# Kernel tuning notes

Hardware: AMD Instinct MI355X
Metric: run time of the kernel (lower is better)

Reference implementation:

```python
import jax, jax.numpy as jnp
import numpy as np

B, L, K, G, C, S = 1024, 32, 8, 8, 128, 32
D_IN = 2 * L + K + S  # masked z (L) + mask (L) + target (K) + shared (S)
TAU = 1.0
EPS = 1e-5
NEG_INF = -1e9  # stands in for torch's -9e15 diagonal fill; sigmoid(-1e9)=0


def setup_inputs() -> dict:
    key = jax.random.key(0)
    ks = jax.random.split(key, 24)
    eye = jnp.eye(K, dtype=bool)
    kaiming = lambda k, shape: jax.random.uniform(k, shape, jnp.float32, -1.0, 1.0) * np.sqrt(6.0 / shape[-1])
    return {
        "z_sample": jax.random.normal(ks[0], (B, L), jnp.float32),
        "target": jax.random.randint(ks[1], (B,), 0, K),
        "z_mean": jax.random.normal(ks[2], (B, L), jnp.float32),
        "z_logstd": 0.1 * jax.random.normal(ks[3], (B, L), jnp.float32),
        "z_shared": jax.random.normal(ks[4], (B, S), jnp.float32),
        "u_gumbel": jax.random.uniform(ks[5], (B, L, K), jnp.float32),
        "u_adj": jax.random.uniform(ks[6], (B, G, K, K), jnp.float32),
        "target_params": 0.1 * jax.random.normal(ks[7], (L, K), jnp.float32),
        "enco_theta": jnp.where(eye, NEG_INF, jax.random.normal(ks[8], (K, K), jnp.float32)),
        "enco_gamma": jnp.where(eye, NEG_INF, jax.random.normal(ks[9], (K, K), jnp.float32)),
        "W1": kaiming(ks[10], (L, C, D_IN)),
        "b1": jnp.zeros((L, C), jnp.float32),
        "gn1_w": jnp.ones((L, C), jnp.float32),
        "gn1_b": jnp.zeros((L, C), jnp.float32),
        "W2": kaiming(ks[11], (L, C, C)),
        "b2": jnp.zeros((L, C), jnp.float32),
        "gn2_w": jnp.ones((L, C), jnp.float32),
        "gn2_b": jnp.zeros((L, C), jnp.float32),
        "W3": 0.01 * jax.random.normal(ks[12], (L, 2, C), jnp.float32),
        "b3": jnp.zeros((L, 2), jnp.float32),
        "tanh_scale": jnp.zeros((L, 2), jnp.float32),
    }


def _mv_linear(x, W, b):
    # x: [B,G,L,d_in], W: [L,d_out,d_in] -> [B,G,L,d_out]  (per-latent independent linear)
    return jnp.einsum("bgld,lhd->bglh", x, W) + b


def _mv_groupnorm(x, w, b):
    # GroupNorm(L groups over L*C channels) == per-(sample, latent) normalization over C
    mu = x.mean(-1, keepdims=True)
    var = ((x - mu) ** 2).mean(-1, keepdims=True)
    return (x - mu) * jax.lax.rsqrt(var + EPS) * w + b


def reference(z_sample, target, z_mean, z_logstd, z_shared, u_gumbel, u_adj,
              target_params, enco_theta, enco_gamma,
              W1, b1, gn1_w, gn1_b, W2, b2, gn2_w, gn2_b, W3, b3, tanh_scale):
    dt = z_sample.dtype
    target_oh = jax.nn.one_hot(target, K, dtype=dt)  # [B,K]

    # hard gumbel-softmax with straight-through estimator: psi assigns latents to causal vars
    g = -jnp.log(-jnp.log(u_gumbel + 1e-10) + 1e-10)
    soft = jax.nn.softmax((target_params[None] + g) / TAU, axis=-1)  # [B,L,K]
    hard = jax.nn.one_hot(jnp.argmax(soft, axis=-1), K, dtype=dt)
    psi = hard + soft - jax.lax.stop_gradient(soft)  # [B,L,K]

    # ENCO graph sampling: edge prob = sigmoid(theta)*sigmoid(gamma), Bernoulli samples
    edge_prob = jax.nn.sigmoid(enco_theta) * jax.nn.sigmoid(enco_gamma)  # [K,K]
    adj = (u_adj < edge_prob[None, None]).astype(dt)  # [B,G,K,K], adj[k,l]=1: k->l

    # latent-level parent mask: mask[b,g,i,j]=1 iff latent j is a parent of latent i
    latent_mask = jnp.einsum("bil,bgkl,bjk->bgij", psi, adj, psi)  # [B,G,L,L]
    latent_mask = latent_mask * (1.0 - jnp.eye(L, dtype=dt))

    # per-latent network input: [masked parents, mask, intervention indicator, shared]
    z_masked = latent_mask * z_sample[:, None, None, :]                        # [B,G,L,L]
    t_inp = jnp.broadcast_to((psi * target_oh[:, None, :])[:, None], (B, G, L, K))
    zs = jnp.broadcast_to(z_shared[:, None, None, :], (B, G, L, S))
    s_inp = jnp.concatenate([z_masked, latent_mask, t_inp, zs], axis=-1)       # [B,G,L,D_IN]

    h = jax.nn.silu(_mv_groupnorm(_mv_linear(s_inp, W1, b1), gn1_w, gn1_b))
    h = jax.nn.silu(_mv_groupnorm(_mv_linear(h, W2, b2), gn2_w, gn2_b))
    h = _mv_linear(h, W3, b3)                                                  # [B,G,L,2]
    sc = jnp.exp(tanh_scale)                                                   # [L,2]
    h = jnp.tanh(h / sc) * sc                                                  # MultivarStableTanh
    prior_mean, prior_logstd = h[..., 0], h[..., 1]                            # [B,G,L]

    # KL(q(z) || p(z)) per latent, averaged over graph samples, summed over latents
    var_q = jnp.exp(2.0 * z_logstd)[:, None]                                   # [B,1,L]
    kld = (prior_logstd - z_logstd[:, None]
           + (var_q + (z_mean[:, None] - prior_mean) ** 2) / (2.0 * jnp.exp(2.0 * prior_logstd))
           - 0.5)                                                              # [B,G,L]
    return kld.mean(axis=1).sum(axis=-1)                                       # [B]
```

## Files before the change

### kernel.cpp

```cpp
#include <hip/hip_runtime.h>
#include <hip/hip_bf16.h>

#define B_DIM 1024
#define L_DIM 32
#define K_DIM 8
#define G_DIM 8
#define C_DIM 128
#define S_DIM 32
#define DIN   104

typedef __bf16  bf16x8 __attribute__((ext_vector_type(8)));
typedef float   f32x4  __attribute__((ext_vector_type(4)));

union frag_u { uint4 u; bf16x8 v; };

static __device__ __forceinline__ unsigned int pk2(float a, float b) {
    __hip_bfloat162 h = __float22bfloat162_rn(make_float2(a, b));
    union { __hip_bfloat162 h; unsigned int u; } v; v.h = h; return v.u;
}
static __device__ __forceinline__ bf16x8 ld_frag(const unsigned short* p) {
    frag_u t; t.u = *(const uint4*)p; return t.v;
}

__global__ __launch_bounds__(256) void prep_kernel(
    const float* __restrict__ u_gumbel,
    const float* __restrict__ u_adj,
    const float* __restrict__ target_params,
    const float* __restrict__ enco_theta,
    const float* __restrict__ enco_gamma,
    const int*   __restrict__ target,
    const float* __restrict__ W1,
    const float* __restrict__ W2,
    float*       __restrict__ out,
    unsigned char* __restrict__ cvarpk,
    unsigned int*  __restrict__ wsmask,
    unsigned short* __restrict__ wscr)
{
    const int t = threadIdx.x;
    if (blockIdx.x >= 1024) {
        int gtid  = (blockIdx.x - 1024) * 256 + t;
        int lane  = gtid & 63;
        int ks    = (gtid >> 6) & 3;
        int mt    = (gtid >> 8) & 3;
        int wm    = (gtid >> 10) & 1;
        int l     = (gtid >> 11) & 31;
        int which = gtid >> 16;
        int m  = 16 * (4 * wm + mt) + (lane & 15);
        int k0 = ks * 32 + (lane >> 4) * 8;
        uint4 o;
        if (which == 0) {
            if (k0 >= 104) {
                o = make_uint4(0u, 0u, 0u, 0u);
            } else {
                const float* p = W1 + (size_t)l * 13312 + m * 104 + k0;
                float4 a = *(const float4*)p, bq = *(const float4*)(p + 4);
                o = make_uint4(pk2(a.x, a.y), pk2(a.z, a.w), pk2(bq.x, bq.y), pk2(bq.z, bq.w));
            }
        } else {
            const float* p = W2 + (size_t)l * 16384 + m * 128 + k0;
            float4 a = *(const float4*)p, bq = *(const float4*)(p + 4);
            o = make_uint4(pk2(a.x, a.y), pk2(a.z, a.w), pk2(bq.x, bq.y), pk2(bq.z, bq.w));
        }
        *(uint4*)(wscr + (size_t)gtid * 8) = o;
        return;
    }

    __shared__ double ep[64];
    __shared__ unsigned char cv8[32];
    __shared__ unsigned long long adjb[8];
    const int b = blockIdx.x;
    if (t < 64) {
        double th = (double)enco_theta[t];
        double ga = (double)enco_gamma[t];
        ep[t] = (1.0 / (1.0 + exp(-th))) * (1.0 / (1.0 + exp(-ga)));
    }
    if (t == 0) out[b] = 0.0f;
    __syncthreads();

    {
        const int l = t >> 3, k = t & 7;
        double u = (double)u_gumbel[b * 256 + t];
        double g = -log(-log(u + 1e-10) + 1e-10);
        double v = (double)target_params[t] + g;
        int bk = k;
        #pragma unroll
        for (int off = 1; off < 8; off <<= 1) {
            double ov = __shfl_xor(v, off, 64);
            int   obk = __shfl_xor(bk, off, 64);
            if (ov > v || (ov == v && obk < bk)) { v = ov; bk = obk; }
        }
        if (k == 0) {
            int tg = target[b];
            unsigned char pkd = (unsigned char)(bk | ((bk == tg) ? 8 : 0));
            cvarpk[b * 32 + l] = pkd;
            cv8[l] = pkd;
        }
    }
    {
        const int wv = t >> 6, lane = t & 63;
        #pragma unroll
        for (int q = 0; q < 2; ++q) {
            int gg = wv + 4 * q;
            double u = (double)u_adj[b * 512 + gg * 64 + lane];
            unsigned long long m = __ballot(u < ep[lane]);
            if (lane == 0) adjb[gg] = m;
        }
    }
    __syncthreads();

    {
        const int g = t >> 5, l = t & 31;
        int lam = cv8[l] & 7;
        unsigned long long bits = adjb[g] >> lam;
        unsigned int mask = 0u;
        #pragma unroll
        for (int j = 0; j < 32; ++j) {
            int kap = cv8[j] & 7;
            mask |= ((unsigned int)(bits >> (kap * 8)) & 1u) << j;
        }
        mask &= ~(1u << l);
        wsmask[l * 8192 + b * 8 + g] = mask;
    }
}

__global__ __launch_bounds__(256, 2) void fused_kernel(
    const float* __restrict__ z_sample,
    const float* __restrict__ z_mean,
    const float* __restrict__ z_logstd,
    const float* __restrict__ z_shared,
    const float* __restrict__ pb1,
    const float* __restrict__ g1w,
    const float* __restrict__ g1b,
    const float* __restrict__ pb2,
    const float* __restrict__ g2w,
    const float* __restrict__ g2b,
    const float* __restrict__ W3,
    const float* __restrict__ pb3,
    const float* __restrict__ tsc,
    const unsigned short* __restrict__ wscr,
    const unsigned char*  __restrict__ cvarpk,
    const unsigned int*   __restrict__ wsmask,
    float* __restrict__ out)
{
    __shared__ __align__(16) unsigned short XH[128][136];
    __shared__ float2 gnA[2][128];
    __shared__ float2 gnB[2][128];
    __shared__ float p_g1w[128], p_g1b[128], p_g2w[128], p_g2b[128], p_b1[128], p_b2[128];
    __shared__ float p_w3[2][128];
    __shared__ float p_b3[2], p_ts[2];
    __shared__ __align__(16) unsigned long long cvs[16][4];

    const int tid  = threadIdx.x;
    const int w    = tid >> 6, lane = tid & 63;
    const int lo   = lane & 15, hi = lane >> 4;
    const int wm   = w & 1, wn = w >> 1;
    const int l    = blockIdx.x & 31;
    const int grp  = blockIdx.x >> 5;

    const unsigned short* w1s = wscr + (size_t)((l * 2 + wm) * 16) * 512 + lane * 8;
    const unsigned short* w2s = wscr + (size_t)(((32 + l) * 2 + wm) * 16) * 512 + lane * 8;

    if (tid < 128) {
        int c = tid;
        p_g1w[c] = g1w[l * 128 + c];  p_g1b[c] = g1b[l * 128 + c];
        p_b1[c]  = pb1[l * 128 + c];  p_w3[0][c] = W3[l * 256 + c];
    } else {
        int c = tid - 128;
        p_g2w[c] = g2w[l * 128 + c];  p_g2b[c] = g2b[l * 128 + c];
        p_b2[c]  = pb2[l * 128 + c];  p_w3[1][c] = W3[l * 256 + 128 + c];
    }
    if (tid == 0) {
        p_b3[0] = pb3[l * 2];  p_b3[1] = pb3[l * 2 + 1];
        p_ts[0] = tsc[l * 2];  p_ts[1] = tsc[l * 2 + 1];
    }
    if (tid < 32)
        ((uint4*)cvs)[tid] = ((const uint4*)(cvarpk + (size_t)grp * 16 * 32))[tid];
    __syncthreads();

    const float inv128 = 1.0f / 128.0f;

    {
        int r  = tid & 127;
        int bl = r >> 3;
        int bg = grp * 16 + bl;
        if (tid < 128) {
            unsigned int m32 = wsmask[l * 8192 + (size_t)bg * 8 + (r & 7)];
            const float4* zp = (const float4*)(z_sample + bg * 32);
            #pragma unroll
            for (int wq = 0; wq < 4; ++wq) {
                float4 a = zp[2 * wq], bq = zp[2 * wq + 1];
                unsigned int mq = m32 >> (wq * 8);
                bool mm[8];
                #pragma unroll
                for (int jb = 0; jb < 8; ++jb) mm[jb] = (mq >> jb) & 1u;
                uint4 xm, xk;
                xm.x = pk2(mm[0] ? a.x : 0.f, mm[1] ? a.y : 0.f);
                xm.y = pk2(mm[2] ? a.z : 0.f, mm[3] ? a.w : 0.f);
                xm.z = pk2(mm[4] ? bq.x : 0.f, mm[5] ? bq.y : 0.f);
                xm.w = pk2(mm[6] ? bq.z : 0.f, mm[7] ? bq.w : 0.f);
                xk.x = (mm[0] ? 0x3F80u : 0u) | (mm[1] ? 0x3F800000u : 0u);
                xk.y = (mm[2] ? 0x3F80u : 0u) | (mm[3] ? 0x3F800000u : 0u);
                xk.z = (mm[4] ? 0x3F80u : 0u) | (mm[5] ? 0x3F800000u : 0u);
                xk.w = (mm[6] ? 0x3F80u : 0u) | (mm[7] ? 0x3F800000u : 0u);
                *(uint4*)&XH[r][wq * 8]      = xm;
                *(uint4*)&XH[r][32 + wq * 8] = xk;
            }
        } else {
            unsigned long long lamB = cvs[bl][l >> 3] >> (8 * (l & 7));
            int lam = (int)(lamB & 7);
            int tf  = (int)(lamB >> 3) & 1;
            union { uint4 u; unsigned short s[8]; } tv;
            #pragma unroll
            for (int kk = 0; kk < 8; ++kk)
                tv.s[kk] = (tf && kk == lam) ? (unsigned short)0x3F80 : (unsigned short)0;
            *(uint4*)&XH[r][64] = tv.u;
            const float4* sp = (const float4*)(z_shared + bg * 32);
            #pragma unroll
            for (int q = 0; q < 4; ++q) {
                float4 a = sp[2 * q], b = sp[2 * q + 1];
                *(uint4*)&XH[r][72 + 8 * q] =
                    make_uint4(pk2(a.x, a.y), pk2(a.z, a.w), pk2(b.x, b.y), pk2(b.z, b.w));
            }
            uint4 zz = make_uint4(0u, 0u, 0u, 0u);
            *(uint4*)&XH[r][104] = zz;
            *(uint4*)&XH[r][112] = zz;
            *(uint4*)&XH[r][120] = zz;
        }
    }
    __syncthreads();

    f32x4 accr[4][4];
    #pragma unroll
    for (int a = 0; a < 4; ++a)
        #pragma unroll
        for (int bq = 0; bq < 4; ++bq) accr[a][bq] = (f32x4){0.f, 0.f, 0.f, 0.f};
    {
        bf16x8 wfr[4];
        #pragma unroll
        for (int mt = 0; mt < 4; ++mt) wfr[mt] = ld_frag(w1s + (mt * 4 + 0) * 512);
        #pragma unroll
        for (int ks = 0; ks < 4; ++ks) {
            bf16x8 bfr[4];
            #pragma unroll
            for (int nt = 0; nt < 4; ++nt)
                bfr[nt] = ld_frag(&XH[16 * (4 * wn + nt) + lo][ks * 32 + hi * 8]);
            bf16x8 wnx[4];
            if (ks < 3) {
                #pragma unroll
                for (int mt = 0; mt < 4; ++mt)
                    wnx[mt] = ld_frag(w1s + (mt * 4 + ks + 1) * 512);
            }
            #pragma unroll
            for (int mt = 0; mt < 4; ++mt)
                #pragma unroll
                for (int nt = 0; nt < 4; ++nt)
                    accr[mt][nt] = __builtin_amdgcn_mfma_f32_16x16x32_bf16(
                        wfr[mt], bfr[nt], accr[mt][nt], 0, 0, 0);
            if (ks < 3) {
                #pragma unroll
                for (int mt = 0; mt < 4; ++mt) wfr[mt] = wnx[mt];
            }
        }
    }

    float s1[4] = {0, 0, 0, 0}, s2[4] = {0, 0, 0, 0};
    #pragma unroll
    for (int mt = 0; mt < 4; ++mt) {
        int cb = 16 * (4 * wm + mt) + 4 * hi;
        #pragma unroll
        for (int rg = 0; rg < 4; ++rg) {
            float bias = p_b1[cb + rg];
            #pragma unroll
            for (int nt = 0; nt < 4; ++nt) {
                float v = accr[mt][nt][rg] + bias;
                accr[mt][nt][rg] = v;
                s1[nt] += v; s2[nt] += v * v;
            }
        }
    }
    #pragma unroll
    for (int nt = 0; nt < 4; ++nt) {
        s1[nt] += __shfl_xor(s1[nt], 16, 64);  s1[nt] += __shfl_xor(s1[nt], 32, 64);
        s2[nt] += __shfl_xor(s2[nt], 16, 64);  s2[nt] += __shfl_xor(s2[nt], 32, 64);
    }
    if (hi == 0) {
        #pragma unroll
        for (int nt = 0; nt < 4; ++nt)
            gnA[wm][16 * (4 * wn + nt) + lo] = make_float2(s1[nt], s2[nt]);
    }
    __syncthreads();

    float mu[4], rstd[4];
    #pragma unroll
    for (int nt = 0; nt < 4; ++nt) {
        float2 a0 = gnA[0][16 * (4 * wn + nt) + lo];
        float2 a1 = gnA[1][16 * (4 * wn + nt) + lo];
        float m_  = (a0.x + a1.x) * inv128;
        float var = (a0.y + a1.y) * inv128 - m_ * m_;
        mu[nt] = m_;  rstd[nt] = rsqrtf(var + 1e-5f);
    }
    #pragma unroll
    for (int mt = 0; mt < 4; ++mt) {
        int cb = 16 * (4 * wm + mt) + 4 * hi;
        #pragma unroll
        for (int nt = 0; nt < 4; ++nt) {
            int n = 16 * (4 * wn + nt) + lo;
            float sl[4];
            #pragma unroll
            for (int rg = 0; rg < 4; ++rg) {
                int c = cb + rg;
                float x = (accr[mt][nt][rg] - mu[nt]) * rstd[nt] * p_g1w[c] + p_g1b[c];
                sl[rg]  = __fdividef(x, 1.0f + __expf(-x));
            }
            *(uint2*)&XH[n][cb] = make_uint2(pk2(sl[0], sl[1]), pk2(sl[2], sl[3]));
        }
    }
    __syncthreads();

    #pragma unroll
    for (int a = 0; a < 4; ++a)
        #pragma unroll
        for (int bq = 0; bq < 4; ++bq) accr[a][bq] = (f32x4){0.f, 0.f, 0.f, 0.f};
    {
        bf16x8 wfr[4];
        #pragma unroll
        for (int mt = 0; mt < 4; ++mt) wfr[mt] = ld_frag(w2s + (mt * 4 + 0) * 512);
        #pragma unroll
        for (int ks = 0; ks < 4; ++ks) {
            bf16x8 bfr[4];
            #pragma unroll
            for (int nt = 0; nt < 4; ++nt)
                bfr[nt] = ld_frag(&XH[16 * (4 * wn + nt) + lo][ks * 32 + hi * 8]);
            bf16x8 wnx[4];
            if (ks < 3) {
                #pragma unroll
                for (int mt = 0; mt < 4; ++mt)
                    wnx[mt] = ld_frag(w2s + (mt * 4 + ks + 1) * 512);
            }
            #pragma unroll
            for (int mt = 0; mt < 4; ++mt)
                #pragma unroll
                for (int nt = 0; nt < 4; ++nt)
                    accr[mt][nt] = __builtin_amdgcn_mfma_f32_16x16x32_bf16(
                        wfr[mt], bfr[nt], accr[mt][nt], 0, 0, 0);
            if (ks < 3) {
                #pragma unroll
                for (int mt = 0; mt < 4; ++mt) wfr[mt] = wnx[mt];
            }
        }
    }

    float t1[4] = {0, 0, 0, 0}, t2[4] = {0, 0, 0, 0};
    #pragma unroll
    for (int mt = 0; mt < 4; ++mt) {
        int cb = 16 * (4 * wm + mt) + 4 * hi;
        #pragma unroll
        for (int rg = 0; rg < 4; ++rg) {
            float bias = p_b2[cb + rg];
            #pragma unroll
            for (int nt = 0; nt < 4; ++nt) {
                float v = accr[mt][nt][rg] + bias;
                accr[mt][nt][rg] = v;
                t1[nt] += v; t2[nt] += v * v;
            }
        }
    }
    #pragma unroll
    for (int nt = 0; nt < 4; ++nt) {
        t1[nt] += __shfl_xor(t1[nt], 16, 64);  t1[nt] += __shfl_xor(t1[nt], 32, 64);
        t2[nt] += __shfl_xor(t2[nt], 16, 64);  t2[nt] += __shfl_xor(t2[nt], 32, 64);
    }
    if (hi == 0) {
        #pragma unroll
        for (int nt = 0; nt < 4; ++nt)
            gnA[wm][16 * (4 * wn + nt) + lo] = make_float2(t1[nt], t2[nt]);
    }
    __syncthreads();

    float pmp[4] = {0, 0, 0, 0}, plp[4] = {0, 0, 0, 0};
    float mu2[4], rstd2[4];
    #pragma unroll
    for (int nt = 0; nt < 4; ++nt) {
        float2 a0 = gnA[0][16 * (4 * wn + nt) + lo];
        float2 a1 = gnA[1][16 * (4 * wn + nt) + lo];
        float m_  = (a0.x + a1.x) * inv128;
        float var = (a0.y + a1.y) * inv128 - m_ * m_;
        mu2[nt] = m_;  rstd2[nt] = rsqrtf(var + 1e-5f);
    }
    #pragma unroll
    for (int mt = 0; mt < 4; ++mt) {
        int cb = 16 * (4 * wm + mt) + 4 * hi;
        #pragma unroll
        for (int rg = 0; rg < 4; ++rg) {
            int c = cb + rg;
            float wg = p_g2w[c], bgn = p_g2b[c], w30 = p_w3[0][c], w31 = p_w3[1][c];
            #pragma unroll
            for (int nt = 0; nt < 4; ++nt) {
                float x  = (accr[mt][nt][rg] - mu2[nt]) * rstd2[nt] * wg + bgn;
                float sl = __fdividef(x, 1.0f + __expf(-x));
                pmp[nt] += sl * w30;
                plp[nt] += sl * w31;
            }
        }
    }
    #pragma unroll
    for (int nt = 0; nt < 4; ++nt) {
        pmp[nt] += __shfl_xor(pmp[nt], 16, 64);  pmp[nt] += __shfl_xor(pmp[nt], 32, 64);
        plp[nt] += __shfl_xor(plp[nt], 16, 64);  plp[nt] += __shfl_xor(plp[nt], 32, 64);
    }
    if (hi == 0) {
        #pragma unroll
        for (int nt = 0; nt < 4; ++nt)
            gnB[wm][16 * (4 * wn + nt) + lo] = make_float2(pmp[nt], plp[nt]);
    }
    __syncthreads();

    if (wm == 0 && hi == 0) {
        float sc0 = __expf(p_ts[0]), sc1 = __expf(p_ts[1]);
        #pragma unroll
        for (int nt = 0; nt < 4; ++nt) {
            int n = 16 * (4 * wn + nt) + lo;
            float2 q0 = gnB[0][n], q1 = gnB[1][n];
            float pm = q0.x + q1.x + p_b3[0];
            float pl = q0.y + q1.y + p_b3[1];
            pm = tanhf(pm / sc0) * sc0;
            pl = tanhf(pl / sc1) * sc1;
            int bg = grp * 16 + (n >> 3);
            float zm = z_mean[bg * 32 + l];
            float zl = z_logstd[bg * 32 + l];
            float vq = __expf(2.0f * zl);
            float d  = zm - pm;
            float kld = pl - zl + (vq + d * d) * 0.5f * __expf(-2.0f * pl) - 0.5f;
            kld += __shfl_xor(kld, 1, 64);
            kld += __shfl_xor(kld, 2, 64);
            kld += __shfl_xor(kld, 4, 64);
            if ((lo & 7) == 0) atomicAdd(&out[bg], kld * 0.125f);
        }
    }
}

extern "C" void kernel_launch(void* const* d_in, const int* in_sizes, int n_in,
                              void* d_out, int out_size, void* d_ws, size_t ws_size,
                              hipStream_t stream) {
    const float* z_sample      = (const float*)d_in[0];
    const int*   target        = (const int*)d_in[1];
    const float* z_mean        = (const float*)d_in[2];
    const float* z_logstd      = (const float*)d_in[3];
    const float* z_shared      = (const float*)d_in[4];
    const float* u_gumbel      = (const float*)d_in[5];
    const float* u_adj         = (const float*)d_in[6];
    const float* target_params = (const float*)d_in[7];
    const float* enco_theta    = (const float*)d_in[8];
    const float* enco_gamma    = (const float*)d_in[9];
    const float* W1            = (const float*)d_in[10];
    const float* pb1           = (const float*)d_in[11];
    const float* g1w           = (const float*)d_in[12];
    const float* g1b           = (const float*)d_in[13];
    const float* W2            = (const float*)d_in[14];
    const float* pb2           = (const float*)d_in[15];
    const float* g2w           = (const float*)d_in[16];
    const float* g2b           = (const float*)d_in[17];
    const float* W3            = (const float*)d_in[18];
    const float* pb3           = (const float*)d_in[19];
    const float* tsc           = (const float*)d_in[20];

    unsigned char* cvarpk = (unsigned char*)d_ws;
    unsigned int*  wsmask = (unsigned int*)((char*)d_ws + 32768);
    unsigned short* wscr  = (unsigned short*)((char*)d_ws + 32768 + 1048576);

    prep_kernel<<<1536, 256, 0, stream>>>(u_gumbel, u_adj, target_params,
                                          enco_theta, enco_gamma, target,
                                          W1, W2, (float*)d_out,
                                          cvarpk, wsmask, wscr);
    fused_kernel<<<2048, 256, 0, stream>>>(z_sample, z_mean, z_logstd, z_shared,
                                           pb1, g1w, g1b, pb2, g2w, g2b,
                                           W3, pb3, tsc, wscr, cvarpk, wsmask,
                                           (float*)d_out);
}
```

Baseline: 180.0 us.

## Give each wave full channel tiles to drop cross-wave GroupNorm syncs

Each wave now owns 32 rows and all 128 output channels instead of splitting channels across two waves, so GroupNorm statistics and the W3 projection reduce with intra-wave shuffles rather than shared-memory exchanges and block barriers. The first-layer input fragments are built directly in registers, and the layer-1 activations go to a per-wave LDS slice, which removes the block-wide XH staging and most __syncthreads. In exchange each wave loads the full weight set, doubling per-wave global and L2 weight traffic, and holds 8x2 accumulators in registers. The final tanh is also replaced by an exp-based formula.

```diff
diff --git a/kernel.cpp b/kernel.cpp
--- a/kernel.cpp
+++ b/kernel.cpp
@@ -20,6 +20,12 @@
 }
 static __device__ __forceinline__ bf16x8 ld_frag(const unsigned short* p) {
     frag_u t; t.u = *(const uint4*)p; return t.v;
+}
+static __device__ __forceinline__ bf16x8 u2f(uint4 u) {
+    frag_u t; t.u = u; return t.v;
+}
+static __device__ __forceinline__ float siluf(float x) {
+    return __fdividef(x, 1.0f + __expf(-x));
 }
 
 __global__ __launch_bounds__(256) void prep_kernel(
@@ -142,290 +148,233 @@
     const unsigned int*   __restrict__ wsmask,
     float* __restrict__ out)
 {
-    __shared__ __align__(16) unsigned short XH[128][136];
-    __shared__ float2 gnA[2][128];
-    __shared__ float2 gnB[2][128];
-    __shared__ float p_g1w[128], p_g1b[128], p_g2w[128], p_g2b[128], p_b1[128], p_b2[128];
+    __shared__ __align__(16) unsigned short XH[4][32][136];
+    __shared__ float p_g1w[128], p_g1b[128], p_b1[128];
+    __shared__ float p_g2w[128], p_g2b[128], p_b2[128];
     __shared__ float p_w3[2][128];
     __shared__ float p_b3[2], p_ts[2];
-    __shared__ __align__(16) unsigned long long cvs[16][4];
+    __shared__ unsigned int  msk[128];
+    __shared__ unsigned char cvl[16];
 
     const int tid  = threadIdx.x;
     const int w    = tid >> 6, lane = tid & 63;
     const int lo   = lane & 15, hi = lane >> 4;
-    const int wm   = w & 1, wn = w >> 1;
     const int l    = blockIdx.x & 31;
     const int grp  = blockIdx.x >> 5;
-
-    const unsigned short* w1s = wscr + (size_t)((l * 2 + wm) * 16) * 512 + lane * 8;
-    const unsigned short* w2s = wscr + (size_t)(((32 + l) * 2 + wm) * 16) * 512 + lane * 8;
 
     if (tid < 128) {
         int c = tid;
         p_g1w[c] = g1w[l * 128 + c];  p_g1b[c] = g1b[l * 128 + c];
         p_b1[c]  = pb1[l * 128 + c];  p_w3[0][c] = W3[l * 256 + c];
+        msk[c]   = wsmask[l * 8192 + grp * 128 + c];
     } else {
         int c = tid - 128;
         p_g2w[c] = g2w[l * 128 + c];  p_g2b[c] = g2b[l * 128 + c];
         p_b2[c]  = pb2[l * 128 + c];  p_w3[1][c] = W3[l * 256 + 128 + c];
     }
+    if (tid < 16) cvl[tid] = cvarpk[(size_t)(grp * 16 + tid) * 32 + l];
     if (tid == 0) {
         p_b3[0] = pb3[l * 2];  p_b3[1] = pb3[l * 2 + 1];
         p_ts[0] = tsc[l * 2];  p_ts[1] = tsc[l * 2 + 1];
     }
-    if (tid < 32)
-        ((uint4*)cvs)[tid] = ((const uint4*)(cvarpk + (size_t)grp * 16 * 32))[tid];
     __syncthreads();
 
-    const float inv128 = 1.0f / 128.0f;
-
-    {
-        int r  = tid & 127;
+    bf16x8 bq[2][4];
+    #pragma unroll
+    for (int nt = 0; nt < 2; ++nt) {
+        int r  = w * 32 + nt * 16 + lo;
         int bl = r >> 3;
         int bg = grp * 16 + bl;
-        if (tid < 128) {
-            unsigned int m32 = wsmask[l * 8192 + (size_t)bg * 8 + (r & 7)];
-            const float4* zp = (const float4*)(z_sample + bg * 32);
-            #pragma unroll
-            for (int wq = 0; wq < 4; ++wq) {
-                float4 a = zp[2 * wq], bq = zp[2 * wq + 1];
-                unsigned int mq = m32 >> (wq * 8);
-                bool mm[8];
+        unsigned int m32 = msk[r];
+        unsigned int mq  = (m32 >> (hi * 8)) & 0xffu;
+        const float4* zp = (const float4*)(z_sample + bg * 32 + hi * 8);
+        float4 za = zp[0], zb = zp[1];
+        uint4 f0;
+        f0.x = pk2((mq & 1u)   ? za.x : 0.f, (mq & 2u)   ? za.y : 0.f);
+        f0.y = pk2((mq & 4u)   ? za.z : 0.f, (mq & 8u)   ? za.w : 0.f);
+        f0.z = pk2((mq & 16u)  ? zb.x : 0.f, (mq & 32u)  ? zb.y : 0.f);
+        f0.w = pk2((mq & 64u)  ? zb.z : 0.f, (mq & 128u) ? zb.w : 0.f);
+        uint4 f1;
+        f1.x = ((mq & 1u)   ? 0x3F80u : 0u) | ((mq & 2u)   ? 0x3F800000u : 0u);
+        f1.y = ((mq & 4u)   ? 0x3F80u : 0u) | ((mq & 8u)   ? 0x3F800000u : 0u);
+        f1.z = ((mq & 16u)  ? 0x3F80u : 0u) | ((mq & 32u)  ? 0x3F800000u : 0u);
+        f1.w = ((mq & 64u)  ? 0x3F80u : 0u) | ((mq & 128u) ? 0x3F800000u : 0u);
+        unsigned int cb8 = cvl[bl];
+        int lam = cb8 & 7, tf = (cb8 >> 3) & 1;
+        int zsb = (hi == 0) ? 24 : (hi - 1) * 8;
+        const float4* sp = (const float4*)(z_shared + bg * 32 + zsb);
+        float4 sa = sp[0], sb = sp[1];
+        uint4 fz;
+        fz.x = pk2(sa.x, sa.y); fz.y = pk2(sa.z, sa.w);
+        fz.z = pk2(sb.x, sb.y); fz.w = pk2(sb.z, sb.w);
+        unsigned int ohw = tf ? (0x3F80u << ((lam & 1) << 4)) : 0u;
+        int lq = lam >> 1;
+        uint4 fo;
+        fo.x = (lq == 0) ? ohw : 0u;
+        fo.y = (lq == 1) ? ohw : 0u;
+        fo.z = (lq == 2) ? ohw : 0u;
+        fo.w = (lq == 3) ? ohw : 0u;
+        bool h0 = (hi == 0);
+        uint4 f2, f3;
+        f2.x = h0 ? fo.x : fz.x;  f2.y = h0 ? fo.y : fz.y;
+        f2.z = h0 ? fo.z : fz.z;  f2.w = h0 ? fo.w : fz.w;
+        f3.x = h0 ? fz.x : 0u;    f3.y = h0 ? fz.y : 0u;
+        f3.z = h0 ? fz.z : 0u;    f3.w = h0 ? fz.w : 0u;
+        bq[nt][0] = u2f(f0); bq[nt][1] = u2f(f1);
+        bq[nt][2] = u2f(f2); bq[nt][3] = u2f(f3);
+    }
+
+    const float inv128 = 1.0f / 128.0f;
+
+    f32x4 acc[8][2];
+    #pragma unroll
+    for (int cb = 0; cb < 8; ++cb)
+        #pragma unroll
+        for (int nt = 0; nt < 2; ++nt) acc[cb][nt] = (f32x4){0.f, 0.f, 0.f, 0.f};
+    {
+        const unsigned short* w1p = wscr + (size_t)(l * 32) * 512 + lane * 8;
+        #pragma unroll
+        for (int ks = 0; ks < 4; ++ks) {
+            bf16x8 wf[8];
+            #pragma unroll
+            for (int cb = 0; cb < 8; ++cb) wf[cb] = ld_frag(w1p + (cb * 4 + ks) * 512);
+            #pragma unroll
+            for (int cb = 0; cb < 8; ++cb)
                 #pragma unroll
-                for (int jb = 0; jb < 8; ++jb) mm[jb] = (mq >> jb) & 1u;
-                uint4 xm, xk;
-                xm.x = pk2(mm[0] ? a.x : 0.f, mm[1] ? a.y : 0.f);
-                xm.y = pk2(mm[2] ? a.z : 0.f, mm[3] ? a.w : 0.f);
-                xm.z = pk2(mm[4] ? bq.x : 0.f, mm[5] ? bq.y : 0.f);
-                xm.w = pk2(mm[6] ? bq.z : 0.f, mm[7] ? bq.w : 0.f);
-                xk.x = (mm[0] ? 0x3F80u : 0u) | (mm[1] ? 0x3F800000u : 0u);
-                xk.y = (mm[2] ? 0x3F80u : 0u) | (mm[3] ? 0x3F800000u : 0u);
-                xk.z = (mm[4] ? 0x3F80u : 0u) | (mm[5] ? 0x3F800000u : 0u);
-                xk.w = (mm[6] ? 0x3F80u : 0u) | (mm[7] ? 0x3F800000u : 0u);
-                *(uint4*)&XH[r][wq * 8]      = xm;
-                *(uint4*)&XH[r][32 + wq * 8] = xk;
-            }
-        } else {
-            unsigned long long lamB = cvs[bl][l >> 3] >> (8 * (l & 7));
-            int lam = (int)(lamB & 7);
-            int tf  = (int)(lamB >> 3) & 1;
-            union { uint4 u; unsigned short s[8]; } tv;
-            #pragma unroll
-            for (int kk = 0; kk < 8; ++kk)
-                tv.s[kk] = (tf && kk == lam) ? (unsigned short)0x3F80 : (unsigned short)0;
-            *(uint4*)&XH[r][64] = tv.u;
-            const float4* sp = (const float4*)(z_shared + bg * 32);
-            #pragma unroll
-            for (int q = 0; q < 4; ++q) {
-                float4 a = sp[2 * q], b = sp[2 * q + 1];
-                *(uint4*)&XH[r][72 + 8 * q] =
-                    make_uint4(pk2(a.x, a.y), pk2(a.z, a.w), pk2(b.x, b.y), pk2(b.z, b.w));
-            }
-            uint4 zz = make_uint4(0u, 0u, 0u, 0u);
-            *(uint4*)&XH[r][104] = zz;
-            *(uint4*)&XH[r][112] = zz;
-            *(uint4*)&XH[r][120] = zz;
-        }
-    }
-    __syncthreads();
-
-    f32x4 accr[4][4];
-    #pragma unroll
-    for (int a = 0; a < 4; ++a)
-        #pragma unroll
-        for (int bq = 0; bq < 4; ++bq) accr[a][bq] = (f32x4){0.f, 0.f, 0.f, 0.f};
-    {
-        bf16x8 wfr[4];
-        #pragma unroll
-        for (int mt = 0; mt < 4; ++mt) wfr[mt] = ld_frag(w1s + (mt * 4 + 0) * 512);
-        #pragma unroll
-        for (int ks = 0; ks < 4; ++ks) {
-            bf16x8 bfr[4];
-            #pragma unroll
-            for (int nt = 0; nt < 4; ++nt)
-                bfr[nt] = ld_frag(&XH[16 * (4 * wn + nt) + lo][ks * 32 + hi * 8]);
-            bf16x8 wnx[4];
-            if (ks < 3) {
-                #pragma unroll
-                for (int mt = 0; mt < 4; ++mt)
-                    wnx[mt] = ld_frag(w1s + (mt * 4 + ks + 1) * 512);
-            }
-            #pragma unroll
-            for (int mt = 0; mt < 4; ++mt)
-                #pragma unroll
-                for (int nt = 0; nt < 4; ++nt)
-                    accr[mt][nt] = __builtin_amdgcn_mfma_f32_16x16x32_bf16(
-                        wfr[mt], bfr[nt], accr[mt][nt], 0, 0, 0);
-            if (ks < 3) {
-                #pragma unroll
-                for (int mt = 0; mt < 4; ++mt) wfr[mt] = wnx[mt];
-            }
-        }
-    }
-
-    float s1[4] = {0, 0, 0, 0}, s2[4] = {0, 0, 0, 0};
-    #pragma unroll
-    for (int mt = 0; mt < 4; ++mt) {
-        int cb = 16 * (4 * wm + mt) + 4 * hi;
+                for (int nt = 0; nt < 2; ++nt)
+                    acc[cb][nt] = __builtin_amdgcn_mfma_f32_16x16x32_bf16(
+                        wf[cb], bq[nt][ks], acc[cb][nt], 0, 0, 0);
+        }
+    }
+
+    float s1[2] = {0.f, 0.f}, s2[2] = {0.f, 0.f};
+    #pragma unroll
+    for (int cb = 0; cb < 8; ++cb) {
+        float4 b4 = *(const float4*)&p_b1[cb * 16 + hi * 4];
         #pragma unroll
         for (int rg = 0; rg < 4; ++rg) {
-            float bias = p_b1[cb + rg];
-            #pragma unroll
-            for (int nt = 0; nt < 4; ++nt) {
-                float v = accr[mt][nt][rg] + bias;
-                accr[mt][nt][rg] = v;
-                s1[nt] += v; s2[nt] += v * v;
-            }
-        }
-    }
-    #pragma unroll
-    for (int nt = 0; nt < 4; ++nt) {
+            float bias = ((const float*)&b4)[rg];
+            #pragma unroll
+            for (int nt = 0; nt < 2; ++nt) {
+                float v = acc[cb][nt][rg] + bias;
+                acc[cb][nt][rg] = v;
+                s1[nt] += v;  s2[nt] += v * v;
+            }
+        }
+    }
+    float mu[2], rstd[2];
+    #pragma unroll
+    for (int nt = 0; nt < 2; ++nt) {
         s1[nt] += __shfl_xor(s1[nt], 16, 64);  s1[nt] += __shfl_xor(s1[nt], 32, 64);
         s2[nt] += __shfl_xor(s2[nt], 16, 64);  s2[nt] += __shfl_xor(s2[nt], 32, 64);
-    }
-    if (hi == 0) {
-        #pragma unroll
-        for (int nt = 0; nt < 4; ++nt)
-            gnA[wm][16 * (4 * wn + nt) + lo] = make_float2(s1[nt], s2[nt]);
-    }
-    __syncthreads();
-
-    float mu[4], rstd[4];
-    #pragma unroll
-    for (int nt = 0; nt < 4; ++nt) {
-        float2 a0 = gnA[0][16 * (4 * wn + nt) + lo];
-        float2 a1 = gnA[1][16 * (4 * wn + nt) + lo];
-        float m_  = (a0.x + a1.x) * inv128;
-        float var = (a0.y + a1.y) * inv128 - m_ * m_;
+        float m_  = s1[nt] * inv128;
+        float var = s2[nt] * inv128 - m_ * m_;
         mu[nt] = m_;  rstd[nt] = rsqrtf(var + 1e-5f);
     }
     #pragma unroll
-    for (int mt = 0; mt < 4; ++mt) {
-        int cb = 16 * (4 * wm + mt) + 4 * hi;
-        #pragma unroll
-        for (int nt = 0; nt < 4; ++nt) {
-            int n = 16 * (4 * wn + nt) + lo;
+    for (int cb = 0; cb < 8; ++cb) {
+        float4 gw4 = *(const float4*)&p_g1w[cb * 16 + hi * 4];
+        float4 gb4 = *(const float4*)&p_g1b[cb * 16 + hi * 4];
+        #pragma unroll
+        for (int nt = 0; nt < 2; ++nt) {
             float sl[4];
             #pragma unroll
             for (int rg = 0; rg < 4; ++rg) {
-                int c = cb + rg;
-                float x = (accr[mt][nt][rg] - mu[nt]) * rstd[nt] * p_g1w[c] + p_g1b[c];
-                sl[rg]  = __fdividef(x, 1.0f + __expf(-x));
-            }
-            *(uint2*)&XH[n][cb] = make_uint2(pk2(sl[0], sl[1]), pk2(sl[2], sl[3]));
-        }
-    }
-    __syncthreads();
-
-    #pragma unroll
-    for (int a = 0; a < 4; ++a)
-        #pragma unroll
-        for (int bq = 0; bq < 4; ++bq) accr[a][bq] = (f32x4){0.f, 0.f, 0.f, 0.f};
-    {
-        bf16x8 wfr[4];
-        #pragma unroll
-        for (int mt = 0; mt < 4; ++mt) wfr[mt] = ld_frag(w2s + (mt * 4 + 0) * 512);
+                float x = (acc[cb][nt][rg] - mu[nt]) * rstd[nt] * ((const float*)&gw4)[rg]
+                          + ((const float*)&gb4)[rg];
+                sl[rg] = siluf(x);
+            }
+            *(uint2*)&XH[w][nt * 16 + lo][cb * 16 + hi * 4] =
+                make_uint2(pk2(sl[0], sl[1]), pk2(sl[2], sl[3]));
+        }
+    }
+
+    #pragma unroll
+    for (int cb = 0; cb < 8; ++cb)
+        #pragma unroll
+        for (int nt = 0; nt < 2; ++nt) acc[cb][nt] = (f32x4){0.f, 0.f, 0.f, 0.f};
+    {
+        const unsigned short* w2p = wscr + (size_t)((32 + l) * 32) * 512 + lane * 8;
         #pragma unroll
         for (int ks = 0; ks < 4; ++ks) {
-            bf16x8 bfr[4];
-            #pragma unroll
-            for (int nt = 0; nt < 4; ++nt)
-                bfr[nt] = ld_frag(&XH[16 * (4 * wn + nt) + lo][ks * 32 + hi * 8]);
-            bf16x8 wnx[4];
-            if (ks < 3) {
-                #pragma unroll
-                for (int mt = 0; mt < 4; ++mt)
-                    wnx[mt] = ld_frag(w2s + (mt * 4 + ks + 1) * 512);
-            }
-            #pragma unroll
-            for (int mt = 0; mt < 4; ++mt)
-                #pragma unroll
-                for (int nt = 0; nt < 4; ++nt)
-                    accr[mt][nt] = __builtin_amdgcn_mfma_f32_16x16x32_bf16(
-                        wfr[mt], bfr[nt], accr[mt][nt], 0, 0, 0);
-            if (ks < 3) {
-                #pragma unroll
-                for (int mt = 0; mt < 4; ++mt) wfr[mt] = wnx[mt];
-            }
-        }
-    }
-
-    float t1[4] = {0, 0, 0, 0}, t2[4] = {0, 0, 0, 0};
-    #pragma unroll
-    for (int mt = 0; mt < 4; ++mt) {
-        int cb = 16 * (4 * wm + mt) + 4 * hi;
+            bf16x8 wf[8];
+            #pragma unroll
+            for (int cb = 0; cb < 8; ++cb) wf[cb] = ld_frag(w2p + (cb * 4 + ks) * 512);
+            bf16x8 bf0 = ld_frag(&XH[w][lo][ks * 32 + hi * 8]);
+            bf16x8 bf1 = ld_frag(&XH[w][16 + lo][ks * 32 + hi * 8]);
+            #pragma unroll
+            for (int cb = 0; cb < 8; ++cb) {
+                acc[cb][0] = __builtin_amdgcn_mfma_f32_16x16x32_bf16(
+                    wf[cb], bf0, acc[cb][0], 0, 0, 0);
+                acc[cb][1] = __builtin_amdgcn_mfma_f32_16x16x32_bf16(
+                    wf[cb], bf1, acc[cb][1], 0, 0, 0);
+            }
+        }
+    }
+
+    float t1[2] = {0.f, 0.f}, t2[2] = {0.f, 0.f};
+    #pragma unroll
+    for (int cb = 0; cb < 8; ++cb) {
+        float4 b4 = *(const float4*)&p_b2[cb * 16 + hi * 4];
         #pragma unroll
         for (int rg = 0; rg < 4; ++rg) {
-            float bias = p_b2[cb + rg];
-            #pragma unroll
-            for (int nt = 0; nt < 4; ++nt) {
-                float v = accr[mt][nt][rg] + bias;
-                accr[mt][nt][rg] = v;
-                t1[nt] += v; t2[nt] += v * v;
-            }
-        }
-    }
-    #pragma unroll
-    for (int nt = 0; nt < 4; ++nt) {
+            float bias = ((const float*)&b4)[rg];
+            #pragma unroll
+            for (int nt = 0; nt < 2; ++nt) {
+                float v = acc[cb][nt][rg] + bias;
+                acc[cb][nt][rg] = v;
+                t1[nt] += v;  t2[nt] += v * v;
+            }
+        }
+    }
+    float mu2[2], rstd2[2];
+    #pragma unroll
+    for (int nt = 0; nt < 2; ++nt) {
         t1[nt] += __shfl_xor(t1[nt], 16, 64);  t1[nt] += __shfl_xor(t1[nt], 32, 64);
         t2[nt] += __shfl_xor(t2[nt], 16, 64);  t2[nt] += __shfl_xor(t2[nt], 32, 64);
-    }
-    if (hi == 0) {
-        #pragma unroll
-        for (int nt = 0; nt < 4; ++nt)
-            gnA[wm][16 * (4 * wn + nt) + lo] = make_float2(t1[nt], t2[nt]);
-    }
-    __syncthreads();
-
-    float pmp[4] = {0, 0, 0, 0}, plp[4] = {0, 0, 0, 0};
-    float mu2[4], rstd2[4];
-    #pragma unroll
-    for (int nt = 0; nt < 4; ++nt) {
-        float2 a0 = gnA[0][16 * (4 * wn + nt) + lo];
-        float2 a1 = gnA[1][16 * (4 * wn + nt) + lo];
-        float m_  = (a0.x + a1.x) * inv128;
-        float var = (a0.y + a1.y) * inv128 - m_ * m_;
+        float m_  = t1[nt] * inv128;
+        float var = t2[nt] * inv128 - m_ * m_;
         mu2[nt] = m_;  rstd2[nt] = rsqrtf(var + 1e-5f);
     }
-    #pragma unroll
-    for (int mt = 0; mt < 4; ++mt) {
-        int cb = 16 * (4 * wm + mt) + 4 * hi;
+    float pmp[2] = {0.f, 0.f}, plp[2] = {0.f, 0.f};
+    #pragma unroll
+    for (int cb = 0; cb < 8; ++cb) {
+        float4 gw4 = *(const float4*)&p_g2w[cb * 16 + hi * 4];
+        float4 gb4 = *(const float4*)&p_g2b[cb * 16 + hi * 4];
+        float4 w04 = *(const float4*)&p_w3[0][cb * 16 + hi * 4];
+        float4 w14 = *(const float4*)&p_w3[1][cb * 16 + hi * 4];
         #pragma unroll
         for (int rg = 0; rg < 4; ++rg) {
-            int c = cb + rg;
-            float wg = p_g2w[c], bgn = p_g2b[c], w30 = p_w3[0][c], w31 = p_w3[1][c];
-            #pragma unroll
-            for (int nt = 0; nt < 4; ++nt) {
-                float x  = (accr[mt][nt][rg] - mu2[nt]) * rstd2[nt] * wg + bgn;
-                float sl = __fdividef(x, 1.0f + __expf(-x));
-                pmp[nt] += sl * w30;
-                plp[nt] += sl * w31;
-            }
-        }
-    }
-    #pragma unroll
-    for (int nt = 0; nt < 4; ++nt) {
+            float wg = ((const float*)&gw4)[rg], gb = ((const float*)&gb4)[rg];
+            float w0 = ((const float*)&w04)[rg], w1 = ((const float*)&w14)[rg];
+            #pragma unroll
+            for (int nt = 0; nt < 2; ++nt) {
+                float x  = (acc[cb][nt][rg] - mu2[nt]) * rstd2[nt] * wg + gb;
+                float sl = siluf(x);
+                pmp[nt] += sl * w0;
+                plp[nt] += sl * w1;
+            }
+        }
+    }
+    #pragma unroll
+    for (int nt = 0; nt < 2; ++nt) {
         pmp[nt] += __shfl_xor(pmp[nt], 16, 64);  pmp[nt] += __shfl_xor(pmp[nt], 32, 64);
         plp[nt] += __shfl_xor(plp[nt], 16, 64);  plp[nt] += __shfl_xor(plp[nt], 32, 64);
     }
-    if (hi == 0) {
-        #pragma unroll
-        for (int nt = 0; nt < 4; ++nt)
-            gnB[wm][16 * (4 * wn + nt) + lo] = make_float2(pmp[nt], plp[nt]);
-    }
-    __syncthreads();
-
-    if (wm == 0 && hi == 0) {
+
+    {
         float sc0 = __expf(p_ts[0]), sc1 = __expf(p_ts[1]);
-        #pragma unroll
-        for (int nt = 0; nt < 4; ++nt) {
-            int n = 16 * (4 * wn + nt) + lo;
-            float2 q0 = gnB[0][n], q1 = gnB[1][n];
-            float pm = q0.x + q1.x + p_b3[0];
-            float pl = q0.y + q1.y + p_b3[1];
-            pm = tanhf(pm / sc0) * sc0;
-            pl = tanhf(pl / sc1) * sc1;
-            int bg = grp * 16 + (n >> 3);
+        float is0 = __expf(-p_ts[0]), is1 = __expf(-p_ts[1]);
+        #pragma unroll
+        for (int nt = 0; nt < 2; ++nt) {
+            float pm = pmp[nt] + p_b3[0];
+            float pl = plp[nt] + p_b3[1];
+            float e0 = __expf(2.0f * pm * is0);
+            pm = (1.0f - 2.0f * __fdividef(1.0f, e0 + 1.0f)) * sc0;
+            float e1 = __expf(2.0f * pl * is1);
+            pl = (1.0f - 2.0f * __fdividef(1.0f, e1 + 1.0f)) * sc1;
+            int r  = w * 32 + nt * 16 + lo;
+            int bg = grp * 16 + (r >> 3);
             float zm = z_mean[bg * 32 + l];
             float zl = z_logstd[bg * 32 + l];
             float vq = __expf(2.0f * zl);
@@ -434,7 +383,7 @@
             kld += __shfl_xor(kld, 1, 64);
             kld += __shfl_xor(kld, 2, 64);
             kld += __shfl_xor(kld, 4, 64);
-            if ((lo & 7) == 0) atomicAdd(&out[bg], kld * 0.125f);
+            if (hi == 0 && (lo & 7) == 0) atomicAdd(&out[bg], kld * 0.125f);
         }
     }
 }
```

New measurement: 175.1 us. -2.8%, faster.
